# Kernel optimization log

Hardware: AMD Instinct MI355X
Metric: run time of the kernel (lower is better)

## Reference

```python
import jax, jax.numpy as jnp
import numpy as np

EMBED, HEADS, LEVELS, POINTS = 256, 8, 4, 4
HD = EMBED // HEADS
BS, NQ = 2, 16384
SHAPES = [(128, 128), (64, 64), (32, 32), (16, 16)]  # (H, W) per level
NV = sum(h * w for h, w in SHAPES)
EPS = 1e-5


def layernorm(x, g, b):
    mu = jnp.mean(x, -1, keepdims=True)
    var = jnp.mean((x - mu) ** 2, -1, keepdims=True)
    return (x - mu) / jnp.sqrt(var + EPS) * g + b


def bilinear_sample(vl, loc, H, W):
    # vl: (bs, heads, H*W, hd); loc: (bs, nq, heads, P, 2) normalized [0,1]
    # grid_sample semantics: align_corners=False, zero padding
    x = loc[..., 0] * W - 0.5
    y = loc[..., 1] * H - 0.5
    x0 = jnp.floor(x)
    y0 = jnp.floor(y)
    lx, ly = x - x0, y - y0
    x0 = x0.astype(jnp.int32)
    y0 = y0.astype(jnp.int32)
    gather = jax.vmap(jax.vmap(lambda t, i: t[i]))  # over (bs, heads)
    acc = None
    for dx, dy, w in ((0, 0, (1 - lx) * (1 - ly)), (1, 0, lx * (1 - ly)),
                      (0, 1, (1 - lx) * ly), (1, 1, lx * ly)):
        xi, yi = x0 + dx, y0 + dy
        valid = ((xi >= 0) & (xi < W) & (yi >= 0) & (yi < H)).astype(vl.dtype)
        idx = jnp.clip(yi, 0, H - 1) * W + jnp.clip(xi, 0, W - 1)
        idx = idx.transpose(0, 2, 1, 3)           # (bs, heads, nq, P)
        g = gather(vl, idx)                       # (bs, heads, nq, P, hd)
        wv = (w * valid).transpose(0, 2, 1, 3)[..., None]
        acc = g * wv if acc is None else acc + g * wv
    return acc


def forward(lidar_feat, feat_flatten, ref_2d, spatial_shapes, level_start_index,
            q_pose, W_off, b_off, W_attn, b_attn, W_val, b_val, W_out, b_out,
            ln1_g, ln1_b, ffn_w1, ffn_w2, ln2_g, ln2_b):
    identity = lidar_feat                         # (nq, bs, C)
    q = (lidar_feat + q_pose).transpose(1, 0, 2)  # (bs, nq, C)
    bs, nq, C = q.shape
    v = feat_flatten.transpose(1, 0, 2) @ W_val + b_val
    v = v.reshape(bs, -1, HEADS, HD)
    off = (q @ W_off + b_off).reshape(bs, nq, HEADS, LEVELS, POINTS, 2)
    aw = (q @ W_attn + b_attn).reshape(bs, nq, HEADS, LEVELS * POINTS)
    aw = jax.nn.softmax(aw, -1).reshape(bs, nq, HEADS, LEVELS, POINTS)
    ss = np.asarray(spatial_shapes)               # static level shapes
    lsi = np.asarray(level_start_index)
    norm = jnp.asarray(ss[:, ::-1].copy(), q.dtype)  # (L, 2) [W, H]
    loc = ref_2d[:, :, None, :, None, :] + off / norm[None, None, None, :, None, :]
    out = jnp.zeros((bs, nq, HEADS, HD), q.dtype)
    for l in range(LEVELS):
        H, W = int(ss[l, 0]), int(ss[l, 1])
        s = int(lsi[l])
        vl = v[:, s:s + H * W].transpose(0, 2, 1, 3)   # (bs, heads, HW, hd)
        sampled = bilinear_sample(vl, loc[:, :, :, l], H, W)
        out = out + jnp.einsum('bhqpd,bqhp->bqhd', sampled, aw[:, :, :, l, :])
    out = out.reshape(bs, nq, C) @ W_out + b_out
    out = out.transpose(1, 0, 2) + identity       # residual (dropout=eval noop)
    x = layernorm(out, ln1_g, ln1_b)
    x = layernorm(jnp.maximum(x @ ffn_w1, 0.0) @ ffn_w2 + x, ln2_g, ln2_b)
    return x


def setup_inputs():
    key = jax.random.key(0)
    ks = jax.random.split(key, 16)
    starts = np.cumsum([0] + [h * w for h, w in SHAPES])[:-1]
    d = {
        'lidar_feat': jax.random.normal(ks[0], (NQ, BS, EMBED), jnp.float32),
        'feat_flatten': jax.random.normal(ks[1], (NV, BS, EMBED), jnp.float32),
        'ref_2d': jax.random.uniform(ks[2], (BS, NQ, LEVELS, 2), jnp.float32),
        'spatial_shapes': jnp.array(SHAPES, jnp.int32),
        'level_start_index': jnp.array(starts, jnp.int32),
        'q_pose': jax.random.normal(ks[3], (NQ, BS, EMBED), jnp.float32),
        'W_off': 0.02 * jax.random.normal(ks[4], (EMBED, HEADS * LEVELS * POINTS * 2), jnp.float32),
        'b_off': 2.0 * jax.random.normal(ks[5], (HEADS * LEVELS * POINTS * 2,), jnp.float32),
        'W_attn': 0.02 * jax.random.normal(ks[6], (EMBED, HEADS * LEVELS * POINTS), jnp.float32),
        'b_attn': jnp.zeros((HEADS * LEVELS * POINTS,), jnp.float32),
        'W_val': 0.02 * jax.random.normal(ks[7], (EMBED, EMBED), jnp.float32),
        'b_val': jnp.zeros((EMBED,), jnp.float32),
        'W_out': 0.02 * jax.random.normal(ks[8], (EMBED, EMBED), jnp.float32),
        'b_out': jnp.zeros((EMBED,), jnp.float32),
        'ln1_g': jnp.ones((EMBED,), jnp.float32),
        'ln1_b': jnp.zeros((EMBED,), jnp.float32),
        'ffn_w1': 0.02 * jax.random.normal(ks[9], (EMBED, EMBED), jnp.float32),
        'ffn_w2': 0.02 * jax.random.normal(ks[10], (EMBED, EMBED), jnp.float32),
        'ln2_g': jnp.ones((EMBED,), jnp.float32),
        'ln2_b': jnp.zeros((EMBED,), jnp.float32),
    }
    return d


def reference(lidar_feat, feat_flatten, ref_2d, spatial_shapes, level_start_index,
              q_pose, W_off, b_off, W_attn, b_attn, W_val, b_val, W_out, b_out,
              ln1_g, ln1_b, ffn_w1, ffn_w2, ln2_g, ln2_b):
    return forward(lidar_feat, feat_flatten, ref_2d, spatial_shapes,
                   level_start_index, q_pose, W_off, b_off, W_attn, b_attn,
                   W_val, b_val, W_out, b_out, ln1_g, ln1_b, ffn_w1, ffn_w2,
                   ln2_g, ln2_b)
```

## Files before the change

kernel.cpp:

```cpp
#include <hip/hip_runtime.h>
#include <cstdint>

#define EMBED 256
#define HEADS 8
#define LEVELS 4
#define POINTS 4
#define BS 2
#define NQ 16384
#define NV 21760
#define MQ (BS*NQ)
#define MV (BS*NV)
#define VAL_BLK 340
#define OA_BLK  256

typedef __attribute__((ext_vector_type(8))) short short8;
typedef __attribute__((ext_vector_type(4))) float f32x4;
typedef __attribute__((ext_vector_type(2))) float f32x2;

__device__ __forceinline__ unsigned short f2bf(float f) {
    unsigned int u = __float_as_uint(f);
    u = (u + 0x7FFFu + ((u >> 16) & 1u)) >> 16;
    return (unsigned short)u;
}
__device__ __forceinline__ float bf2f(unsigned short h) {
    return __uint_as_float(((unsigned int)h) << 16);
}
__device__ __forceinline__ void glds16(const unsigned short* g, unsigned short* l) {
    __builtin_amdgcn_global_load_lds((const __attribute__((address_space(1))) void*)g,
                                     (__attribute__((address_space(3))) void*)l, 16, 0, 0);
}

struct WtArgs {
    const float* src[6];
    unsigned short* dst[6];
    int n[6];
};
__global__ __launch_bounds__(256) void prep_wt(
    WtArgs a, const float* __restrict__ ref2d, int* __restrict__ bkt)
{
    const int t = threadIdx.x, g = blockIdx.y, bx = blockIdx.x;
    if (g == 6) {
        if (bx < 64) {
#pragma unroll
            for (int i = 0; i < 2; ++i) {
                const int rb = bx * 512 + i * 256 + t;
                const float x = ref2d[(size_t)rb * 8 + 0];
                const float y = ref2d[(size_t)rb * 8 + 1];
                const int qx = min(15, max(0, (int)(x * 16.f)));
                const int qy = min(15, max(0, (int)(y * 16.f)));
                bkt[rb] = (rb >> 14) * 256 + qy * 16 + qx;
            }
        }
        return;
    }
    const int N = a.n[g];
    const int e = bx * 256 + t;
    if (e >= 256 * N) return;
    const int k = e / N, n = e - k * N;
    a.dst[g][(size_t)n * 256 + k] = f2bf(a.src[g][e]);
}

template<int NCOLS>
__device__ __forceinline__ void gemm_core(
    unsigned short* As, unsigned short* Bs, int bx,
    const float* __restrict__ Af, const float* __restrict__ A2f, int inner,
    const unsigned short* __restrict__ Bt,
    const float* __restrict__ bias0, const float* __restrict__ bias1,
    unsigned short* __restrict__ lidarb, unsigned short* __restrict__ outh)
{
    constexpr int FN = NCOLS / 64;
    const int t = threadIdx.x, l = t & 63, w = t >> 6;
    const int wm = w >> 2, wn = w & 3;
    const int frow = l & 15, fgrp = l >> 4;
    const size_t brow = (size_t)bx * 128;

    const int fslot = fgrp ^ ((frow & 3) ^ ((frow >> 2) & 3));
    const int srow = l >> 2;
    const int sswz = (l & 3) ^ ((srow & 3) ^ ((srow >> 2) & 3));
    const unsigned short* gB0 = Bt + ((size_t)(w * 16 + srow)) * 256 + sswz * 8;

    const int arow_s = t >> 2, aslot_s = t & 3;
    const int grow = (int)brow + arow_s;
    const int bidx = grow / inner, nn = grow - bidx * inner;
    const size_t srcrow = (size_t)(nn * BS + bidx) * 256;
    const float* srcA = Af + srcrow;
    const float* srcA2 = A2f ? A2f + srcrow : nullptr;
    const int aswz_s = aslot_s ^ ((arow_s & 3) ^ ((arow_s >> 2) & 3));

    f32x4 acc[4][FN];
#pragma unroll
    for (int i = 0; i < 4; ++i)
#pragma unroll
        for (int j = 0; j < FN; ++j) acc[i][j] = f32x4{0.f, 0.f, 0.f, 0.f};

    float4 pA0 = *(const float4*)(srcA + aslot_s * 8);
    float4 pA1 = *(const float4*)(srcA + aslot_s * 8 + 4);
    float4 pC0, pC1;
    if (srcA2) { pC0 = *(const float4*)(srcA2 + aslot_s * 8);
                 pC1 = *(const float4*)(srcA2 + aslot_s * 8 + 4); }

    for (int k0 = 0; k0 < 256; k0 += 32) {
        glds16(gB0 + k0,         &Bs[w * 512]);
        glds16(gB0 + 32768 + k0, &Bs[(w + 8) * 512]);
        if constexpr (NCOLS == 384)
            glds16(gB0 + 65536 + k0, &Bs[(w + 16) * 512]);

        if (lidarb) {
            short8 lk;
            lk[0] = (short)f2bf(pA0.x); lk[1] = (short)f2bf(pA0.y);
            lk[2] = (short)f2bf(pA0.z); lk[3] = (short)f2bf(pA0.w);
            lk[4] = (short)f2bf(pA1.x); lk[5] = (short)f2bf(pA1.y);
            lk[6] = (short)f2bf(pA1.z); lk[7] = (short)f2bf(pA1.w);
            *reinterpret_cast<short8*>(lidarb + srcrow + k0 + aslot_s * 8) = lk;
        }

        float c[8] = {pA0.x, pA0.y, pA0.z, pA0.w, pA1.x, pA1.y, pA1.z, pA1.w};
        if (srcA2) {
            c[0] += pC0.x; c[1] += pC0.y; c[2] += pC0.z; c[3] += pC0.w;
            c[4] += pC1.x; c[5] += pC1.y; c[6] += pC1.z; c[7] += pC1.w;
        }
        short8 pk;
#pragma unroll
        for (int i = 0; i < 8; ++i) pk[i] = (short)f2bf(c[i]);
        *reinterpret_cast<short8*>(&As[arow_s * 32 + aswz_s * 8]) = pk;
        if (k0 + 32 < 256) {
            pA0 = *(const float4*)(srcA + k0 + 32 + aslot_s * 8);
            pA1 = *(const float4*)(srcA + k0 + 32 + aslot_s * 8 + 4);
            if (srcA2) { pC0 = *(const float4*)(srcA2 + k0 + 32 + aslot_s * 8);
                         pC1 = *(const float4*)(srcA2 + k0 + 32 + aslot_s * 8 + 4); }
        }
        __syncthreads();

        short8 af[4]; short8 bq[FN];
#pragma unroll
        for (int fm = 0; fm < 4; ++fm)
            af[fm] = *reinterpret_cast<const short8*>(&As[(wm * 64 + fm * 16 + frow) * 32 + fslot * 8]);
#pragma unroll
        for (int fn = 0; fn < FN; ++fn)
            bq[fn] = *reinterpret_cast<const short8*>(&Bs[(wn * (NCOLS / 4) + fn * 16 + frow) * 32 + fslot * 8]);
#pragma unroll
        for (int fm = 0; fm < 4; ++fm)
#pragma unroll
            for (int fn = 0; fn < FN; ++fn)
                acc[fm][fn] = __builtin_amdgcn_mfma_f32_16x16x32_bf16(af[fm], bq[fn], acc[fm][fn], 0, 0, 0);
        __syncthreads();
    }

#pragma unroll
    for (int fn = 0; fn < FN; ++fn) {
        const int col = wn * (NCOLS / 4) + fn * 16 + frow;
        float b = 0.f;
        if (NCOLS == 384) b = (col < 256) ? bias0[col] : bias1[col - 256];
        else              b = bias0[col];
#pragma unroll
        for (int fm = 0; fm < 4; ++fm)
#pragma unroll
            for (int j = 0; j < 4; ++j) {
                const size_t row = brow + wm * 64 + fm * 16 + fgrp * 4 + j;
                outh[row * NCOLS + col] = f2bf(acc[fm][fn][j] + b);
            }
    }
}

__global__ __launch_bounds__(512) void valoa_k(
    const float* __restrict__ feat, const float* __restrict__ lidar,
    const float* __restrict__ q_pose,
    const unsigned short* __restrict__ wt_val, const unsigned short* __restrict__ wt_oa,
    const float* __restrict__ b_val, const float* __restrict__ b_off,
    const float* __restrict__ b_attn,
    unsigned short* __restrict__ vb, unsigned short* __restrict__ oa,
    unsigned short* __restrict__ lidarb,
    const int* __restrict__ bkt, int* __restrict__ perm)
{
    __shared__ unsigned short As[128 * 32];
    __shared__ unsigned short Bs[384 * 32];
    const int bx = blockIdx.x;
    if (bx < VAL_BLK) {
        gemm_core<256>(As, Bs, bx, feat, nullptr, NV, wt_val, b_val, nullptr, nullptr, vb);
    } else if (bx < VAL_BLK + OA_BLK) {
        gemm_core<384>(As, Bs, bx - VAL_BLK, lidar, q_pose, NQ, wt_oa, b_off, b_attn, lidarb, oa);
    } else {
        int* hcnt = (int*)As;
        int* cur  = ((int*)As) + 512;
        int* s    = (int*)Bs;
        const int t = threadIdx.x;
        hcnt[t] = 0;
        __syncthreads();
#pragma unroll 4
        for (int i = 0; i < 64; ++i) atomicAdd(&hcnt[bkt[i * 512 + t]], 1);
        __syncthreads();
        const int v = hcnt[t];
        s[t] = v;
        __syncthreads();
        int acc = v;
#pragma unroll
        for (int o = 1; o < 512; o <<= 1) {
            const int add = (t >= o) ? s[t - o] : 0;
            __syncthreads();
            acc += add;
            s[t] = acc;
            __syncthreads();
        }
        cur[t] = acc - v;
        __syncthreads();
#pragma unroll 4
        for (int i = 0; i < 64; ++i) {
            const int rb = i * 512 + t;
            const int pos = atomicAdd(&cur[bkt[rb]], 1);
            perm[pos] = rb;
        }
    }
}

__global__ __launch_bounds__(256) void sampler_k(
    const unsigned short* __restrict__ oa,
    const float* __restrict__ ref2d,
    const unsigned short* __restrict__ v,
    const int* __restrict__ perm,
    unsigned short* __restrict__ outh)
{
    const int bid = blockIdx.x;
    const int sbid = (bid & 7) * (MQ / 4 / 8) + (bid >> 3);
    const int q0 = sbid * 4;
    const int t = threadIdx.x;

    __shared__ __align__(16) uint2 s_d[4][8][74];

#pragma unroll
    for (int it = 0; it < 2; ++it) {
        const int item = t + it * 256;
        const int tq = item >> 7, hlp = item & 127;
        const int h = hlp >> 4, lp = hlp & 15, li = lp >> 2;
        const int rb = perm[q0 + tq];
        const int b = rb >> 14;

        const float2 refv = *(const float2*)(ref2d + (size_t)rb * 8 + li * 2);
        const ushort2 offu = *(const ushort2*)(oa + (size_t)rb * 384 + hlp * 2);
        const float ax = bf2f(oa[(size_t)rb * 384 + 256 + hlp]);

        float m = ax;
#pragma unroll
        for (int o = 1; o < 16; o <<= 1) m = fmaxf(m, __shfl_xor(m, o));
        const float e = __expf(ax - m);
        float sden = e;
#pragma unroll
        for (int o = 1; o < 16; o <<= 1) sden += __shfl_xor(sden, o);
        const float a = e / sden;

        const int Wl[4]  = {128, 64, 32, 16};
        const int S0l[4] = {0, 16384, 20480, 21504};
        const int Wi = Wl[li]; const float Wf = (float)Wi;
        const float x = (refv.x + bf2f(offu.x) / Wf) * Wf - 0.5f;
        const float y = (refv.y + bf2f(offu.y) / Wf) * Wf - 0.5f;
        const float x0f = floorf(x), y0f = floorf(y);
        const float lx = x - x0f, ly = y - y0f;
        const int x0 = (int)x0f, y0 = (int)y0f;
        const float cw[4] = {(1.f - lx) * (1.f - ly) * a, lx * (1.f - ly) * a,
                             (1.f - lx) * ly * a,          lx * ly * a};
        const int base = b * NV + S0l[li];
#pragma unroll
        for (int c = 0; c < 4; ++c) {
            const int xi = x0 + (c & 1), yi = y0 + (c >> 1);
            const bool val = (xi >= 0) & (xi < Wi) & (yi >= 0) & (yi < Wi);
            const int xc = min(max(xi, 0), Wi - 1), yc = min(max(yi, 0), Wi - 1);
            const unsigned int ofs = (unsigned int)(base + yc * Wi + xc) * 256u + h * 32;
            s_d[tq][h][c * 18 + lp] = make_uint2(__float_as_uint(val ? cw[c] : 0.f), ofs);
        }
    }
    __syncthreads();

    const int tq = t >> 6, l = t & 63, h = l >> 3, dq = l & 7;
    const int rb = perm[q0 + tq], b = rb >> 14, qi = rb & (NQ - 1);
    const unsigned short* vd = v + dq * 4;
    const uint2* dp = &s_d[tq][h][0];
    f32x2 acc01 = {0.f, 0.f}, acc23 = {0.f, 0.f};
#pragma unroll
    for (int c = 0; c < 4; ++c) {
#pragma unroll
        for (int i = 0; i < 8; ++i) {
            const uint4 dd = *(const uint4*)(dp + c * 18 + i * 2);
            {
                const uint2 raw = *(const uint2*)(vd + dd.y);
                const float w0 = __uint_as_float(dd.x);
                f32x2 v01; v01.x = __uint_as_float(raw.x << 16);
                           v01.y = __uint_as_float(raw.x & 0xFFFF0000u);
                f32x2 v23; v23.x = __uint_as_float(raw.y << 16);
                           v23.y = __uint_as_float(raw.y & 0xFFFF0000u);
                acc01 += w0 * v01;
                acc23 += w0 * v23;
            }
            {
                const uint2 raw = *(const uint2*)(vd + dd.w);
                const float w1 = __uint_as_float(dd.z);
                f32x2 v01; v01.x = __uint_as_float(raw.x << 16);
                           v01.y = __uint_as_float(raw.x & 0xFFFF0000u);
                f32x2 v23; v23.x = __uint_as_float(raw.y << 16);
                           v23.y = __uint_as_float(raw.y & 0xFFFF0000u);
                acc01 += w1 * v01;
                acc23 += w1 * v23;
            }
        }
    }
    ushort4 o;
    o.x = f2bf(acc01.x); o.y = f2bf(acc01.y);
    o.z = f2bf(acc23.x); o.w = f2bf(acc23.y);
    *(ushort4*)(outh + (size_t)(qi * BS + b) * 256 + h * 32 + dq * 4) = o;
}

__global__ __launch_bounds__(512) void outproj_k(
    const unsigned short* __restrict__ smp, const unsigned short* __restrict__ lidarb,
    const unsigned short* __restrict__ Wo, const float* __restrict__ b_out,
    const float* __restrict__ ln1g, const float* __restrict__ ln1b,
    unsigned short* __restrict__ xln)
{
    __shared__ unsigned short As[128 * 32];
    __shared__ unsigned short Bs[256 * 32];
    __shared__ float2 sdLN[128][4];

    const int t = threadIdx.x, l = t & 63, w = t >> 6;
    const int wm = w >> 2, wn = w & 3;
    const int frow = l & 15, fgrp = l >> 4;
    const size_t brow = (size_t)blockIdx.x * 128;

    const int fslot = fgrp ^ ((frow & 3) ^ ((frow >> 2) & 3));
    const int srow = l >> 2;
    const int sswz = (l & 3) ^ ((srow & 3) ^ ((srow >> 2) & 3));

    const unsigned short* gA = smp + (brow + (size_t)(w * 16 + srow)) * 256 + sswz * 8;
    const unsigned short* gB = Wo + ((size_t)(w * 16 + srow)) * 256 + sswz * 8;

    f32x4 acc[4][4];
#pragma unroll
    for (int i = 0; i < 4; ++i)
#pragma unroll
        for (int j = 0; j < 4; ++j) acc[i][j] = f32x4{0.f, 0.f, 0.f, 0.f};

    for (int k0 = 0; k0 < 256; k0 += 32) {
        glds16(gB + k0,         &Bs[w * 512]);
        glds16(gB + 32768 + k0, &Bs[(w + 8) * 512]);
        glds16(gA + k0, &As[w * 512]);
        __syncthreads();

        short8 af[4], bq[4];
#pragma unroll
        for (int fm = 0; fm < 4; ++fm)
            af[fm] = *reinterpret_cast<const short8*>(&As[(wm * 64 + fm * 16 + frow) * 32 + fslot * 8]);
#pragma unroll
        for (int fn = 0; fn < 4; ++fn)
            bq[fn] = *reinterpret_cast<const short8*>(&Bs[(wn * 64 + fn * 16 + frow) * 32 + fslot * 8]);
#pragma unroll
        for (int fm = 0; fm < 4; ++fm)
#pragma unroll
            for (int fn = 0; fn < 4; ++fn)
                acc[fm][fn] = __builtin_amdgcn_mfma_f32_16x16x32_bf16(af[fm], bq[fn], acc[fm][fn], 0, 0, 0);
        __syncthreads();
    }

    int cols[4];
#pragma unroll
    for (int fn = 0; fn < 4; ++fn) cols[fn] = wn * 64 + fn * 16 + frow;

#pragma unroll
    for (int fm = 0; fm < 4; ++fm)
#pragma unroll
        for (int j = 0; j < 4; ++j) {
            const size_t row = brow + wm * 64 + fm * 16 + fgrp * 4 + j;
#pragma unroll
            for (int fn = 0; fn < 4; ++fn)
                acc[fm][fn][j] += b_out[cols[fn]] + bf2f(lidarb[row * 256 + cols[fn]]);
        }

#pragma unroll
    for (int fm = 0; fm < 4; ++fm)
#pragma unroll
        for (int j = 0; j < 4; ++j) {
            float s1 = 0.f, s2 = 0.f;
#pragma unroll
            for (int fn = 0; fn < 4; ++fn) { const float x = acc[fm][fn][j]; s1 += x; s2 += x * x; }
#pragma unroll
            for (int o = 1; o < 16; o <<= 1) { s1 += __shfl_xor(s1, o); s2 += __shfl_xor(s2, o); }
            if (frow == 0)
                sdLN[wm * 64 + fm * 16 + fgrp * 4 + j][wn] = make_float2(s1, s2);
        }
    __syncthreads();
    float gv[4], bv[4];
#pragma unroll
    for (int fn = 0; fn < 4; ++fn) { gv[fn] = ln1g[cols[fn]]; bv[fn] = ln1b[cols[fn]]; }
#pragma unroll
    for (int fm = 0; fm < 4; ++fm)
#pragma unroll
        for (int j = 0; j < 4; ++j) {
            const int rl = wm * 64 + fm * 16 + fgrp * 4 + j;
            const float2 p0 = sdLN[rl][0], p1 = sdLN[rl][1], p2 = sdLN[rl][2], p3 = sdLN[rl][3];
            const float s1 = p0.x + p1.x + p2.x + p3.x;
            const float s2 = p0.y + p1.y + p2.y + p3.y;
            const float mu = s1 * (1.f / 256.f);
            const float var = s2 * (1.f / 256.f) - mu * mu;
            const float rstd = rsqrtf(var + 1e-5f);
            const size_t row = brow + rl;
#pragma unroll
            for (int fn = 0; fn < 4; ++fn)
                xln[row * 256 + cols[fn]] = f2bf((acc[fm][fn][j] - mu) * rstd * gv[fn] + bv[fn]);
        }
}

__global__ __launch_bounds__(512) void ffn_fused(
    const unsigned short* __restrict__ X,
    const unsigned short* __restrict__ W1t, const unsigned short* __restrict__ W2t,
    const float* __restrict__ lng, const float* __restrict__ lnb,
    float* __restrict__ outf)
{
    __shared__ unsigned short As[64 * 32];
    __shared__ unsigned short Bs[256 * 32];
    __shared__ unsigned short Hs[64 * 256];
    __shared__ float2 sdLN[64][4];

    const int t = threadIdx.x, l = t & 63, w = t >> 6;
    const int wm = w >> 2, wn = w & 3;
    const int frow = l & 15, fgrp = l >> 4;
    const size_t brow = (size_t)blockIdx.x * 64;

    const int fslot = fgrp ^ ((frow & 3) ^ ((frow >> 2) & 3));
    const int srow = l >> 2;
    const int sswz = (l & 3) ^ ((srow & 3) ^ ((srow >> 2) & 3));

    const unsigned short* gX  = X + (brow + (size_t)((w & 3) * 16 + srow)) * 256 + sswz * 8;
    const unsigned short* gW1 = W1t + ((size_t)(w * 16 + srow)) * 256 + sswz * 8;
    const unsigned short* gW2 = W2t + ((size_t)(w * 16 + srow)) * 256 + sswz * 8;

    f32x4 acc[2][4];

#pragma unroll
    for (int i = 0; i < 2; ++i)
#pragma unroll
        for (int j = 0; j < 4; ++j) acc[i][j] = f32x4{0.f, 0.f, 0.f, 0.f};

    for (int k0 = 0; k0 < 256; k0 += 32) {
        glds16(gW1 + k0,         &Bs[w * 512]);
        glds16(gW1 + 32768 + k0, &Bs[(w + 8) * 512]);
        if (w < 4) glds16(gX + k0, &As[w * 512]);
        __syncthreads();

        short8 af[2], bq[4];
#pragma unroll
        for (int fm = 0; fm < 2; ++fm)
            af[fm] = *reinterpret_cast<const short8*>(&As[(wm * 32 + fm * 16 + frow) * 32 + fslot * 8]);
#pragma unroll
        for (int fn = 0; fn < 4; ++fn)
            bq[fn] = *reinterpret_cast<const short8*>(&Bs[(wn * 64 + fn * 16 + frow) * 32 + fslot * 8]);
#pragma unroll
        for (int fm = 0; fm < 2; ++fm)
#pragma unroll
            for (int fn = 0; fn < 4; ++fn)
                acc[fm][fn] = __builtin_amdgcn_mfma_f32_16x16x32_bf16(af[fm], bq[fn], acc[fm][fn], 0, 0, 0);
        __syncthreads();
    }

#pragma unroll
    for (int fm = 0; fm < 2; ++fm)
#pragma unroll
        for (int fn = 0; fn < 4; ++fn) {
            const int col = wn * 64 + fn * 16 + frow;
#pragma unroll
            for (int j = 0; j < 4; ++j) {
                const int row = wm * 32 + fm * 16 + fgrp * 4 + j;
                const int ss = (col >> 3) ^ (row & 7);
                Hs[row * 256 + ss * 8 + (col & 7)] = f2bf(fmaxf(acc[fm][fn][j], 0.f));
            }
        }
    __syncthreads();

#pragma unroll
    for (int i = 0; i < 2; ++i)
#pragma unroll
        for (int j = 0; j < 4; ++j) acc[i][j] = f32x4{0.f, 0.f, 0.f, 0.f};

    for (int k0 = 0; k0 < 256; k0 += 32) {
        glds16(gW2 + k0,         &Bs[w * 512]);
        glds16(gW2 + 32768 + k0, &Bs[(w + 8) * 512]);
        __syncthreads();

        short8 af[2], bq[4];
#pragma unroll
        for (int fm = 0; fm < 2; ++fm) {
            const int row = wm * 32 + fm * 16 + frow;
            const int ksg = (k0 >> 3) + fgrp;
            const int ss = ksg ^ (row & 7);
            af[fm] = *reinterpret_cast<const short8*>(&Hs[row * 256 + ss * 8]);
        }
#pragma unroll
        for (int fn = 0; fn < 4; ++fn)
            bq[fn] = *reinterpret_cast<const short8*>(&Bs[(wn * 64 + fn * 16 + frow) * 32 + fslot * 8]);
#pragma unroll
        for (int fm = 0; fm < 2; ++fm)
#pragma unroll
            for (int fn = 0; fn < 4; ++fn)
                acc[fm][fn] = __builtin_amdgcn_mfma_f32_16x16x32_bf16(af[fm], bq[fn], acc[fm][fn], 0, 0, 0);
        __syncthreads();
    }

#pragma unroll
    for (int fm = 0; fm < 2; ++fm)
#pragma unroll
        for (int fn = 0; fn < 4; ++fn) {
            const int col = wn * 64 + fn * 16 + frow;
#pragma unroll
            for (int j = 0; j < 4; ++j) {
                const size_t row = brow + wm * 32 + fm * 16 + fgrp * 4 + j;
                acc[fm][fn][j] += bf2f(X[row * 256 + col]);
            }
        }
#pragma unroll
    for (int fm = 0; fm < 2; ++fm)
#pragma unroll
        for (int j = 0; j < 4; ++j) {
            float s1 = 0.f, s2 = 0.f;
#pragma unroll
            for (int fn = 0; fn < 4; ++fn) { const float x = acc[fm][fn][j]; s1 += x; s2 += x * x; }
#pragma unroll
            for (int o = 1; o < 16; o <<= 1) { s1 += __shfl_xor(s1, o); s2 += __shfl_xor(s2, o); }
            if (frow == 0)
                sdLN[wm * 32 + fm * 16 + fgrp * 4 + j][wn] = make_float2(s1, s2);
        }
    __syncthreads();
#pragma unroll
    for (int fm = 0; fm < 2; ++fm)
#pragma unroll
        for (int j = 0; j < 4; ++j) {
            const int rl = wm * 32 + fm * 16 + fgrp * 4 + j;
            const float2 p0 = sdLN[rl][0], p1 = sdLN[rl][1], p2 = sdLN[rl][2], p3 = sdLN[rl][3];
            const float s1 = p0.x + p1.x + p2.x + p3.x;
            const float s2 = p0.y + p1.y + p2.y + p3.y;
            const float mu = s1 * (1.f / 256.f);
            const float var = s2 * (1.f / 256.f) - mu * mu;
            const float rstd = rsqrtf(var + 1e-5f);
            const size_t row = brow + rl;
#pragma unroll
            for (int fn = 0; fn < 4; ++fn) {
                const int col = wn * 64 + fn * 16 + frow;
                outf[row * 256 + col] = (acc[fm][fn][j] - mu) * rstd * lng[col] + lnb[col];
            }
        }
}

extern "C" void kernel_launch(void* const* d_in, const int* in_sizes, int n_in,
                              void* d_out, int out_size, void* d_ws, size_t ws_size,
                              hipStream_t stream)
{
    const float* lidar  = (const float*)d_in[0];
    const float* feat   = (const float*)d_in[1];
    const float* ref2d  = (const float*)d_in[2];
    const float* q_pose = (const float*)d_in[5];
    const float* W_off  = (const float*)d_in[6];
    const float* b_off  = (const float*)d_in[7];
    const float* W_attn = (const float*)d_in[8];
    const float* b_attn = (const float*)d_in[9];
    const float* W_val  = (const float*)d_in[10];
    const float* b_val  = (const float*)d_in[11];
    const float* W_out  = (const float*)d_in[12];
    const float* b_out  = (const float*)d_in[13];
    const float* ln1_g  = (const float*)d_in[14];
    const float* ln1_b  = (const float*)d_in[15];
    const float* ffn_w1 = (const float*)d_in[16];
    const float* ffn_w2 = (const float*)d_in[17];
    const float* ln2_g  = (const float*)d_in[18];
    const float* ln2_b  = (const float*)d_in[19];

    float* out = (float*)d_out;
    char*  ws  = (char*)d_ws;

    unsigned short* vb     = (unsigned short*)(ws + 0);
    unsigned short* oa     = (unsigned short*)(ws + 22282240);
    unsigned short* smp    = (unsigned short*)(ws + 47448064);
    unsigned short* xln    = (unsigned short*)(ws + 64225280);
    unsigned short* lidarb = (unsigned short*)(ws + 81002496);
    unsigned short* wt     = (unsigned short*)(ws + 97779712);
    int* perm = (int*)(ws + 98500608);
    int* bkt  = (int*)(ws + 98631680);
    unsigned short* wt_val = wt;
    unsigned short* wt_oa  = wt + 65536;
    unsigned short* wt_out = wt + 163840;
    unsigned short* wt_f1  = wt + 229376;
    unsigned short* wt_f2  = wt + 294912;

    WtArgs wa;
    wa.src[0] = W_val;  wa.dst[0] = wt_val;          wa.n[0] = 256;
    wa.src[1] = W_off;  wa.dst[1] = wt_oa;           wa.n[1] = 256;
    wa.src[2] = W_attn; wa.dst[2] = wt_oa + 65536;   wa.n[2] = 128;
    wa.src[3] = W_out;  wa.dst[3] = wt_out;          wa.n[3] = 256;
    wa.src[4] = ffn_w1; wa.dst[4] = wt_f1;           wa.n[4] = 256;
    wa.src[5] = ffn_w2; wa.dst[5] = wt_f2;           wa.n[5] = 256;

    prep_wt<<<dim3(384, 7), dim3(256), 0, stream>>>(wa, ref2d, bkt);

    valoa_k<<<dim3(VAL_BLK + OA_BLK + 1), dim3(512), 0, stream>>>(
        feat, lidar, q_pose, wt_val, wt_oa, b_val, b_off, b_attn,
        vb, oa, lidarb, bkt, perm);

    sampler_k<<<dim3(MQ / 4), dim3(256), 0, stream>>>(oa, ref2d, vb, perm, smp);

    outproj_k<<<dim3(MQ / 128), dim3(512), 0, stream>>>(
        smp, lidarb, wt_out, b_out, ln1_g, ln1_b, xln);

    ffn_fused<<<dim3(MQ / 64), dim3(512), 0, stream>>>(
        xln, wt_f1, wt_f2, ln2_g, ln2_b, out);
}
```

Before: 195.2 us.

## Pre-convert GEMM inputs to bf16 in prep kernel and load A via LDS DMA

Adds a separate pass in the prep kernel that converts feat, lidar and lidar+q_pose to bf16 row-major buffers. This lets the value and offset/attention GEMMs stream A tiles with global_load_lds instead of loading fp32, converting in registers and storing to LDS. The bucket histogram now builds with global atomics during prep, so the single sort block only does the scan and scatter. The cost is an extra full read and write of the inputs in bf16 plus a memset, traded for a simpler, more latency-tolerant GEMM main loop.

```diff
diff --git a/kernel.cpp b/kernel.cpp
--- a/kernel.cpp
+++ b/kernel.cpp
@@ -13,6 +13,11 @@
 #define VAL_BLK 340
 #define OA_BLK  256
 
+#define WT_B  2304
+#define BKT_B 2368
+#define FB_B  13248
+#define QB_B  21440
+
 typedef __attribute__((ext_vector_type(8))) short short8;
 typedef __attribute__((ext_vector_type(4))) float f32x4;
 typedef __attribute__((ext_vector_type(2))) float f32x2;
@@ -35,38 +40,65 @@
     unsigned short* dst[6];
     int n[6];
 };
-__global__ __launch_bounds__(256) void prep_wt(
-    WtArgs a, const float* __restrict__ ref2d, int* __restrict__ bkt)
+__global__ __launch_bounds__(256) void prep_k(
+    WtArgs a, const float* __restrict__ ref2d,
+    const float* __restrict__ feat, const float* __restrict__ lidar,
+    const float* __restrict__ q_pose,
+    unsigned short* __restrict__ featb, unsigned short* __restrict__ qb,
+    unsigned short* __restrict__ lidarb,
+    int* __restrict__ bkt, int* __restrict__ hist)
 {
-    const int t = threadIdx.x, g = blockIdx.y, bx = blockIdx.x;
-    if (g == 6) {
-        if (bx < 64) {
-#pragma unroll
-            for (int i = 0; i < 2; ++i) {
-                const int rb = bx * 512 + i * 256 + t;
-                const float x = ref2d[(size_t)rb * 8 + 0];
-                const float y = ref2d[(size_t)rb * 8 + 1];
-                const int qx = min(15, max(0, (int)(x * 16.f)));
-                const int qy = min(15, max(0, (int)(y * 16.f)));
-                bkt[rb] = (rb >> 14) * 256 + qy * 16 + qx;
-            }
-        }
-        return;
-    }
-    const int N = a.n[g];
-    const int e = bx * 256 + t;
-    if (e >= 256 * N) return;
-    const int k = e / N, n = e - k * N;
-    a.dst[g][(size_t)n * 256 + k] = f2bf(a.src[g][e]);
+    const int bx = blockIdx.x, t = threadIdx.x;
+    if (bx < WT_B) {
+        const int g = bx / 384;
+        const int e = (bx - g * 384) * 256 + t;
+        const int N = a.n[g];
+        if (e < 256 * N) {
+            const int k = e / N, n = e - k * N;
+            a.dst[g][(size_t)n * 256 + k] = f2bf(a.src[g][e]);
+        }
+    } else if (bx < BKT_B) {
+        const int base = (bx - WT_B) * 512;
+#pragma unroll
+        for (int i = 0; i < 2; ++i) {
+            const int rb = base + i * 256 + t;
+            const float x = ref2d[(size_t)rb * 8 + 0];
+            const float y = ref2d[(size_t)rb * 8 + 1];
+            const int qx = min(15, max(0, (int)(x * 16.f)));
+            const int qy = min(15, max(0, (int)(y * 16.f)));
+            const int bv = (rb >> 14) * 256 + qy * 16 + qx;
+            bkt[rb] = bv;
+            atomicAdd(&hist[bv], 1);
+        }
+    } else if (bx < FB_B) {
+        const int r = (bx - BKT_B) * 4 + (t >> 6);
+        const int c = (t & 63) * 4;
+        const int b = r / NV, n = r - b * NV;
+        const float4 v4 = *(const float4*)(feat + (size_t)(n * BS + b) * 256 + c);
+        ushort4 o; o.x = f2bf(v4.x); o.y = f2bf(v4.y); o.z = f2bf(v4.z); o.w = f2bf(v4.w);
+        *(ushort4*)(featb + (size_t)r * 256 + c) = o;
+    } else {
+        const int r = (bx - FB_B) * 4 + (t >> 6);
+        const int c = (t & 63) * 4;
+        const int b = r >> 14, n = r & (NQ - 1);
+        const size_t src = (size_t)(n * BS + b) * 256 + c;
+        const float4 lv = *(const float4*)(lidar + src);
+        const float4 qv = *(const float4*)(q_pose + src);
+        ushort4 lo; lo.x = f2bf(lv.x); lo.y = f2bf(lv.y); lo.z = f2bf(lv.z); lo.w = f2bf(lv.w);
+        *(ushort4*)(lidarb + src) = lo;
+        ushort4 qo;
+        qo.x = f2bf(lv.x + qv.x); qo.y = f2bf(lv.y + qv.y);
+        qo.z = f2bf(lv.z + qv.z); qo.w = f2bf(lv.w + qv.w);
+        *(ushort4*)(qb + (size_t)r * 256 + c) = qo;
+    }
 }
 
 template<int NCOLS>
-__device__ __forceinline__ void gemm_core(
+__device__ __forceinline__ void gemm_bf(
     unsigned short* As, unsigned short* Bs, int bx,
-    const float* __restrict__ Af, const float* __restrict__ A2f, int inner,
-    const unsigned short* __restrict__ Bt,
+    const unsigned short* __restrict__ A, const unsigned short* __restrict__ Bt,
     const float* __restrict__ bias0, const float* __restrict__ bias1,
-    unsigned short* __restrict__ lidarb, unsigned short* __restrict__ outh)
+    unsigned short* __restrict__ outh)
 {
     constexpr int FN = NCOLS / 64;
     const int t = threadIdx.x, l = t & 63, w = t >> 6;
@@ -77,15 +109,9 @@
     const int fslot = fgrp ^ ((frow & 3) ^ ((frow >> 2) & 3));
     const int srow = l >> 2;
     const int sswz = (l & 3) ^ ((srow & 3) ^ ((srow >> 2) & 3));
-    const unsigned short* gB0 = Bt + ((size_t)(w * 16 + srow)) * 256 + sswz * 8;
-
-    const int arow_s = t >> 2, aslot_s = t & 3;
-    const int grow = (int)brow + arow_s;
-    const int bidx = grow / inner, nn = grow - bidx * inner;
-    const size_t srcrow = (size_t)(nn * BS + bidx) * 256;
-    const float* srcA = Af + srcrow;
-    const float* srcA2 = A2f ? A2f + srcrow : nullptr;
-    const int aswz_s = aslot_s ^ ((arow_s & 3) ^ ((arow_s >> 2) & 3));
+
+    const unsigned short* gA = A + (brow + (size_t)(w * 16 + srow)) * 256 + sswz * 8;
+    const unsigned short* gB = Bt + ((size_t)(w * 16 + srow)) * 256 + sswz * 8;
 
     f32x4 acc[4][FN];
 #pragma unroll
@@ -93,42 +119,12 @@
 #pragma unroll
         for (int j = 0; j < FN; ++j) acc[i][j] = f32x4{0.f, 0.f, 0.f, 0.f};
 
-    float4 pA0 = *(const float4*)(srcA + aslot_s * 8);
-    float4 pA1 = *(const float4*)(srcA + aslot_s * 8 + 4);
-    float4 pC0, pC1;
-    if (srcA2) { pC0 = *(const float4*)(srcA2 + aslot_s * 8);
-                 pC1 = *(const float4*)(srcA2 + aslot_s * 8 + 4); }
-
     for (int k0 = 0; k0 < 256; k0 += 32) {
-        glds16(gB0 + k0,         &Bs[w * 512]);
-        glds16(gB0 + 32768 + k0, &Bs[(w + 8) * 512]);
+        glds16(gB + k0,         &Bs[w * 512]);
+        glds16(gB + 32768 + k0, &Bs[(w + 8) * 512]);
         if constexpr (NCOLS == 384)
-            glds16(gB0 + 65536 + k0, &Bs[(w + 16) * 512]);
-
-        if (lidarb) {
-            short8 lk;
-            lk[0] = (short)f2bf(pA0.x); lk[1] = (short)f2bf(pA0.y);
-            lk[2] = (short)f2bf(pA0.z); lk[3] = (short)f2bf(pA0.w);
-            lk[4] = (short)f2bf(pA1.x); lk[5] = (short)f2bf(pA1.y);
-            lk[6] = (short)f2bf(pA1.z); lk[7] = (short)f2bf(pA1.w);
-            *reinterpret_cast<short8*>(lidarb + srcrow + k0 + aslot_s * 8) = lk;
-        }
-
-        float c[8] = {pA0.x, pA0.y, pA0.z, pA0.w, pA1.x, pA1.y, pA1.z, pA1.w};
-        if (srcA2) {
-            c[0] += pC0.x; c[1] += pC0.y; c[2] += pC0.z; c[3] += pC0.w;
-            c[4] += pC1.x; c[5] += pC1.y; c[6] += pC1.z; c[7] += pC1.w;
-        }
-        short8 pk;
-#pragma unroll
-        for (int i = 0; i < 8; ++i) pk[i] = (short)f2bf(c[i]);
-        *reinterpret_cast<short8*>(&As[arow_s * 32 + aswz_s * 8]) = pk;
-        if (k0 + 32 < 256) {
-            pA0 = *(const float4*)(srcA + k0 + 32 + aslot_s * 8);
-            pA1 = *(const float4*)(srcA + k0 + 32 + aslot_s * 8 + 4);
-            if (srcA2) { pC0 = *(const float4*)(srcA2 + k0 + 32 + aslot_s * 8);
-                         pC1 = *(const float4*)(srcA2 + k0 + 32 + aslot_s * 8 + 4); }
-        }
+            glds16(gB + 65536 + k0, &Bs[(w + 16) * 512]);
+        glds16(gA + k0, &As[w * 512]);
         __syncthreads();
 
         short8 af[4]; short8 bq[FN];
@@ -149,7 +145,7 @@
 #pragma unroll
     for (int fn = 0; fn < FN; ++fn) {
         const int col = wn * (NCOLS / 4) + fn * 16 + frow;
-        float b = 0.f;
+        float b;
         if (NCOLS == 384) b = (col < 256) ? bias0[col] : bias1[col - 256];
         else              b = bias0[col];
 #pragma unroll
@@ -163,33 +159,26 @@
 }
 
 __global__ __launch_bounds__(512) void valoa_k(
-    const float* __restrict__ feat, const float* __restrict__ lidar,
-    const float* __restrict__ q_pose,
+    const unsigned short* __restrict__ featb, const unsigned short* __restrict__ qb,
     const unsigned short* __restrict__ wt_val, const unsigned short* __restrict__ wt_oa,
     const float* __restrict__ b_val, const float* __restrict__ b_off,
     const float* __restrict__ b_attn,
     unsigned short* __restrict__ vb, unsigned short* __restrict__ oa,
-    unsigned short* __restrict__ lidarb,
-    const int* __restrict__ bkt, int* __restrict__ perm)
+    const int* __restrict__ hist, const int* __restrict__ bkt,
+    int* __restrict__ perm)
 {
     __shared__ unsigned short As[128 * 32];
     __shared__ unsigned short Bs[384 * 32];
     const int bx = blockIdx.x;
     if (bx < VAL_BLK) {
-        gemm_core<256>(As, Bs, bx, feat, nullptr, NV, wt_val, b_val, nullptr, nullptr, vb);
+        gemm_bf<256>(As, Bs, bx, featb, wt_val, b_val, nullptr, vb);
     } else if (bx < VAL_BLK + OA_BLK) {
-        gemm_core<384>(As, Bs, bx - VAL_BLK, lidar, q_pose, NQ, wt_oa, b_off, b_attn, lidarb, oa);
+        gemm_bf<384>(As, Bs, bx - VAL_BLK, qb, wt_oa, b_off, b_attn, oa);
     } else {
-        int* hcnt = (int*)As;
-        int* cur  = ((int*)As) + 512;
-        int* s    = (int*)Bs;
+        int* s   = (int*)As;
+        int* cur = ((int*)As) + 512;
         const int t = threadIdx.x;
-        hcnt[t] = 0;
-        __syncthreads();
-#pragma unroll 4
-        for (int i = 0; i < 64; ++i) atomicAdd(&hcnt[bkt[i * 512 + t]], 1);
-        __syncthreads();
-        const int v = hcnt[t];
+        const int v = hist[t];
         s[t] = v;
         __syncthreads();
         int acc = v;
@@ -572,11 +561,14 @@
     unsigned short* vb     = (unsigned short*)(ws + 0);
     unsigned short* oa     = (unsigned short*)(ws + 22282240);
     unsigned short* smp    = (unsigned short*)(ws + 47448064);
+    unsigned short* qb     = smp;
     unsigned short* xln    = (unsigned short*)(ws + 64225280);
-    unsigned short* lidarb = (unsigned short*)(ws + 81002496);
-    unsigned short* wt     = (unsigned short*)(ws + 97779712);
-    int* perm = (int*)(ws + 98500608);
-    int* bkt  = (int*)(ws + 98631680);
+    unsigned short* featb  = xln;
+    unsigned short* lidarb = (unsigned short*)(ws + 86507520);
+    unsigned short* wt     = (unsigned short*)(ws + 103284736);
+    int* perm = (int*)(ws + 104005632);
+    int* bkt  = (int*)(ws + 104136704);
+    int* hist = (int*)(ws + 104267776);
     unsigned short* wt_val = wt;
     unsigned short* wt_oa  = wt + 65536;
     unsigned short* wt_out = wt + 163840;
@@ -591,11 +583,14 @@
     wa.src[4] = ffn_w1; wa.dst[4] = wt_f1;           wa.n[4] = 256;
     wa.src[5] = ffn_w2; wa.dst[5] = wt_f2;           wa.n[5] = 256;
 
-    prep_wt<<<dim3(384, 7), dim3(256), 0, stream>>>(wa, ref2d, bkt);
+    hipMemsetAsync(hist, 0, 2048, stream);
+
+    prep_k<<<dim3(QB_B), dim3(256), 0, stream>>>(
+        wa, ref2d, feat, lidar, q_pose, featb, qb, lidarb, bkt, hist);
 
     valoa_k<<<dim3(VAL_BLK + OA_BLK + 1), dim3(512), 0, stream>>>(
-        feat, lidar, q_pose, wt_val, wt_oa, b_val, b_off, b_attn,
-        vb, oa, lidarb, bkt, perm);
+        featb, qb, wt_val, wt_oa, b_val, b_off, b_attn,
+        vb, oa, hist, bkt, perm);
 
     sampler_k<<<dim3(MQ / 4), dim3(256), 0, stream>>>(oa, ref2d, vb, perm, smp);
 
```

New measurement: 211.9 us. +8.6%, slower.

## Shrink value/offset GEMM tiles to 32 rows and precompute bucket histogram

Applied to the files above, without the earlier changes.

The fused value/offset-attention projection GEMM now uses 32-row tiles with 256-thread blocks instead of 128-row tiles with 512 threads. This gives about four times as many blocks for better CU occupancy and load balance. The query bucket histogram moves into the prep kernel via global atomics, so the sort block in valoa_k only runs a prefix scan and scatter. The trade-offs are that B tiles are reloaded by more blocks, the new histogram buffer needs an extra memset, and there is global atomic contention.

```diff
diff --git a/kernel.cpp b/kernel.cpp
--- a/kernel.cpp
+++ b/kernel.cpp
@@ -10,8 +10,8 @@
 #define NV 21760
 #define MQ (BS*NQ)
 #define MV (BS*NV)
-#define VAL_BLK 340
-#define OA_BLK  256
+#define VAL32 1360
+#define OA32  1024
 
 typedef __attribute__((ext_vector_type(8))) short short8;
 typedef __attribute__((ext_vector_type(4))) float f32x4;
@@ -36,7 +36,8 @@
     int n[6];
 };
 __global__ __launch_bounds__(256) void prep_wt(
-    WtArgs a, const float* __restrict__ ref2d, int* __restrict__ bkt)
+    WtArgs a, const float* __restrict__ ref2d,
+    int* __restrict__ bkt, int* __restrict__ hist)
 {
     const int t = threadIdx.x, g = blockIdx.y, bx = blockIdx.x;
     if (g == 6) {
@@ -48,7 +49,9 @@
                 const float y = ref2d[(size_t)rb * 8 + 1];
                 const int qx = min(15, max(0, (int)(x * 16.f)));
                 const int qy = min(15, max(0, (int)(y * 16.f)));
-                bkt[rb] = (rb >> 14) * 256 + qy * 16 + qx;
+                const int bv = (rb >> 14) * 256 + qy * 16 + qx;
+                bkt[rb] = bv;
+                atomicAdd(&hist[bv], 1);
             }
         }
         return;
@@ -61,7 +64,7 @@
 }
 
 template<int NCOLS>
-__device__ __forceinline__ void gemm_core(
+__device__ __forceinline__ void gemm32(
     unsigned short* As, unsigned short* Bs, int bx,
     const float* __restrict__ Af, const float* __restrict__ A2f, int inner,
     const unsigned short* __restrict__ Bt,
@@ -70,76 +73,65 @@
 {
     constexpr int FN = NCOLS / 64;
     const int t = threadIdx.x, l = t & 63, w = t >> 6;
-    const int wm = w >> 2, wn = w & 3;
     const int frow = l & 15, fgrp = l >> 4;
-    const size_t brow = (size_t)bx * 128;
+    const size_t brow = (size_t)bx * 32;
 
     const int fslot = fgrp ^ ((frow & 3) ^ ((frow >> 2) & 3));
     const int srow = l >> 2;
     const int sswz = (l & 3) ^ ((srow & 3) ^ ((srow >> 2) & 3));
     const unsigned short* gB0 = Bt + ((size_t)(w * 16 + srow)) * 256 + sswz * 8;
 
-    const int arow_s = t >> 2, aslot_s = t & 3;
-    const int grow = (int)brow + arow_s;
+    const int arow = t >> 3;
+    const int acol = (t & 7) * 4;
+    const int grow = (int)brow + arow;
     const int bidx = grow / inner, nn = grow - bidx * inner;
     const size_t srcrow = (size_t)(nn * BS + bidx) * 256;
     const float* srcA = Af + srcrow;
     const float* srcA2 = A2f ? A2f + srcrow : nullptr;
-    const int aswz_s = aslot_s ^ ((arow_s & 3) ^ ((arow_s >> 2) & 3));
-
-    f32x4 acc[4][FN];
-#pragma unroll
-    for (int i = 0; i < 4; ++i)
+    const int aslot = (t & 7) >> 1, ahalf = t & 1;
+    const int aswz = aslot ^ ((arow & 3) ^ ((arow >> 2) & 3));
+    const int aoff = arow * 32 + aswz * 8 + ahalf * 4;
+
+    f32x4 acc[2][FN];
+#pragma unroll
+    for (int i = 0; i < 2; ++i)
 #pragma unroll
         for (int j = 0; j < FN; ++j) acc[i][j] = f32x4{0.f, 0.f, 0.f, 0.f};
 
-    float4 pA0 = *(const float4*)(srcA + aslot_s * 8);
-    float4 pA1 = *(const float4*)(srcA + aslot_s * 8 + 4);
-    float4 pC0, pC1;
-    if (srcA2) { pC0 = *(const float4*)(srcA2 + aslot_s * 8);
-                 pC1 = *(const float4*)(srcA2 + aslot_s * 8 + 4); }
+    float4 pA = *(const float4*)(srcA + acol);
+    float4 pC;
+    if (srcA2) pC = *(const float4*)(srcA2 + acol);
 
     for (int k0 = 0; k0 < 256; k0 += 32) {
-        glds16(gB0 + k0,         &Bs[w * 512]);
-        glds16(gB0 + 32768 + k0, &Bs[(w + 8) * 512]);
-        if constexpr (NCOLS == 384)
-            glds16(gB0 + 65536 + k0, &Bs[(w + 16) * 512]);
+#pragma unroll
+        for (int c = 0; c < FN; ++c)
+            glds16(gB0 + c * 16384 + k0, &Bs[(c * 4 + w) * 512]);
 
         if (lidarb) {
-            short8 lk;
-            lk[0] = (short)f2bf(pA0.x); lk[1] = (short)f2bf(pA0.y);
-            lk[2] = (short)f2bf(pA0.z); lk[3] = (short)f2bf(pA0.w);
-            lk[4] = (short)f2bf(pA1.x); lk[5] = (short)f2bf(pA1.y);
-            lk[6] = (short)f2bf(pA1.z); lk[7] = (short)f2bf(pA1.w);
-            *reinterpret_cast<short8*>(lidarb + srcrow + k0 + aslot_s * 8) = lk;
-        }
-
-        float c[8] = {pA0.x, pA0.y, pA0.z, pA0.w, pA1.x, pA1.y, pA1.z, pA1.w};
-        if (srcA2) {
-            c[0] += pC0.x; c[1] += pC0.y; c[2] += pC0.z; c[3] += pC0.w;
-            c[4] += pC1.x; c[5] += pC1.y; c[6] += pC1.z; c[7] += pC1.w;
-        }
-        short8 pk;
-#pragma unroll
-        for (int i = 0; i < 8; ++i) pk[i] = (short)f2bf(c[i]);
-        *reinterpret_cast<short8*>(&As[arow_s * 32 + aswz_s * 8]) = pk;
+            ushort4 lk;
+            lk.x = f2bf(pA.x); lk.y = f2bf(pA.y); lk.z = f2bf(pA.z); lk.w = f2bf(pA.w);
+            *(ushort4*)(lidarb + srcrow + k0 + acol) = lk;
+        }
+        float c0 = pA.x, c1 = pA.y, c2 = pA.z, c3 = pA.w;
+        if (srcA2) { c0 += pC.x; c1 += pC.y; c2 += pC.z; c3 += pC.w; }
+        ushort4 pk; pk.x = f2bf(c0); pk.y = f2bf(c1); pk.z = f2bf(c2); pk.w = f2bf(c3);
+        *(ushort4*)(&As[aoff]) = pk;
+
         if (k0 + 32 < 256) {
-            pA0 = *(const float4*)(srcA + k0 + 32 + aslot_s * 8);
-            pA1 = *(const float4*)(srcA + k0 + 32 + aslot_s * 8 + 4);
-            if (srcA2) { pC0 = *(const float4*)(srcA2 + k0 + 32 + aslot_s * 8);
-                         pC1 = *(const float4*)(srcA2 + k0 + 32 + aslot_s * 8 + 4); }
-        }
-        __syncthreads();
-
-        short8 af[4]; short8 bq[FN];
-#pragma unroll
-        for (int fm = 0; fm < 4; ++fm)
-            af[fm] = *reinterpret_cast<const short8*>(&As[(wm * 64 + fm * 16 + frow) * 32 + fslot * 8]);
+            pA = *(const float4*)(srcA + k0 + 32 + acol);
+            if (srcA2) pC = *(const float4*)(srcA2 + k0 + 32 + acol);
+        }
+        __syncthreads();
+
+        short8 af[2]; short8 bq[FN];
+#pragma unroll
+        for (int fm = 0; fm < 2; ++fm)
+            af[fm] = *reinterpret_cast<const short8*>(&As[(fm * 16 + frow) * 32 + fslot * 8]);
 #pragma unroll
         for (int fn = 0; fn < FN; ++fn)
-            bq[fn] = *reinterpret_cast<const short8*>(&Bs[(wn * (NCOLS / 4) + fn * 16 + frow) * 32 + fslot * 8]);
-#pragma unroll
-        for (int fm = 0; fm < 4; ++fm)
+            bq[fn] = *reinterpret_cast<const short8*>(&Bs[(w * (NCOLS / 4) + fn * 16 + frow) * 32 + fslot * 8]);
+#pragma unroll
+        for (int fm = 0; fm < 2; ++fm)
 #pragma unroll
             for (int fn = 0; fn < FN; ++fn)
                 acc[fm][fn] = __builtin_amdgcn_mfma_f32_16x16x32_bf16(af[fm], bq[fn], acc[fm][fn], 0, 0, 0);
@@ -148,21 +140,21 @@
 
 #pragma unroll
     for (int fn = 0; fn < FN; ++fn) {
-        const int col = wn * (NCOLS / 4) + fn * 16 + frow;
-        float b = 0.f;
+        const int col = w * (NCOLS / 4) + fn * 16 + frow;
+        float b;
         if (NCOLS == 384) b = (col < 256) ? bias0[col] : bias1[col - 256];
         else              b = bias0[col];
 #pragma unroll
-        for (int fm = 0; fm < 4; ++fm)
+        for (int fm = 0; fm < 2; ++fm)
 #pragma unroll
             for (int j = 0; j < 4; ++j) {
-                const size_t row = brow + wm * 64 + fm * 16 + fgrp * 4 + j;
+                const size_t row = brow + fm * 16 + fgrp * 4 + j;
                 outh[row * NCOLS + col] = f2bf(acc[fm][fn][j] + b);
             }
     }
 }
 
-__global__ __launch_bounds__(512) void valoa_k(
+__global__ __launch_bounds__(256) void valoa_k(
     const float* __restrict__ feat, const float* __restrict__ lidar,
     const float* __restrict__ q_pose,
     const unsigned short* __restrict__ wt_val, const unsigned short* __restrict__ wt_oa,
@@ -170,42 +162,40 @@
     const float* __restrict__ b_attn,
     unsigned short* __restrict__ vb, unsigned short* __restrict__ oa,
     unsigned short* __restrict__ lidarb,
-    const int* __restrict__ bkt, int* __restrict__ perm)
+    const int* __restrict__ hist, const int* __restrict__ bkt,
+    int* __restrict__ perm)
 {
-    __shared__ unsigned short As[128 * 32];
+    __shared__ unsigned short As[32 * 32];
     __shared__ unsigned short Bs[384 * 32];
     const int bx = blockIdx.x;
-    if (bx < VAL_BLK) {
-        gemm_core<256>(As, Bs, bx, feat, nullptr, NV, wt_val, b_val, nullptr, nullptr, vb);
-    } else if (bx < VAL_BLK + OA_BLK) {
-        gemm_core<384>(As, Bs, bx - VAL_BLK, lidar, q_pose, NQ, wt_oa, b_off, b_attn, lidarb, oa);
+    if (bx < VAL32) {
+        gemm32<256>(As, Bs, bx, feat, nullptr, NV, wt_val, b_val, nullptr, nullptr, vb);
+    } else if (bx < VAL32 + OA32) {
+        gemm32<384>(As, Bs, bx - VAL32, lidar, q_pose, NQ, wt_oa, b_off, b_attn, lidarb, oa);
     } else {
-        int* hcnt = (int*)As;
-        int* cur  = ((int*)As) + 512;
-        int* s    = (int*)Bs;
+        int* ps  = (int*)As;
+        int* cur = (int*)Bs;
         const int t = threadIdx.x;
-        hcnt[t] = 0;
-        __syncthreads();
-#pragma unroll 4
-        for (int i = 0; i < 64; ++i) atomicAdd(&hcnt[bkt[i * 512 + t]], 1);
-        __syncthreads();
-        const int v = hcnt[t];
-        s[t] = v;
-        __syncthreads();
-        int acc = v;
-#pragma unroll
-        for (int o = 1; o < 512; o <<= 1) {
-            const int add = (t >= o) ? s[t - o] : 0;
+        const int2 hv = ((const int2*)hist)[t];
+        const int pair = hv.x + hv.y;
+        ps[t] = pair;
+        __syncthreads();
+        int acc = pair;
+#pragma unroll
+        for (int o = 1; o < 256; o <<= 1) {
+            const int add = (t >= o) ? ps[t - o] : 0;
             __syncthreads();
             acc += add;
-            s[t] = acc;
+            ps[t] = acc;
             __syncthreads();
         }
-        cur[t] = acc - v;
+        const int excl = acc - pair;
+        cur[2 * t]     = excl;
+        cur[2 * t + 1] = excl + hv.x;
         __syncthreads();
 #pragma unroll 4
-        for (int i = 0; i < 64; ++i) {
-            const int rb = i * 512 + t;
+        for (int i = 0; i < 128; ++i) {
+            const int rb = i * 256 + t;
             const int pos = atomicAdd(&cur[bkt[rb]], 1);
             perm[pos] = rb;
         }
@@ -577,6 +567,7 @@
     unsigned short* wt     = (unsigned short*)(ws + 97779712);
     int* perm = (int*)(ws + 98500608);
     int* bkt  = (int*)(ws + 98631680);
+    int* hist = (int*)(ws + 98762752);
     unsigned short* wt_val = wt;
     unsigned short* wt_oa  = wt + 65536;
     unsigned short* wt_out = wt + 163840;
@@ -591,11 +582,13 @@
     wa.src[4] = ffn_w1; wa.dst[4] = wt_f1;           wa.n[4] = 256;
     wa.src[5] = ffn_w2; wa.dst[5] = wt_f2;           wa.n[5] = 256;
 
-    prep_wt<<<dim3(384, 7), dim3(256), 0, stream>>>(wa, ref2d, bkt);
-
-    valoa_k<<<dim3(VAL_BLK + OA_BLK + 1), dim3(512), 0, stream>>>(
+    hipMemsetAsync(hist, 0, 2048, stream);
+
+    prep_wt<<<dim3(384, 7), dim3(256), 0, stream>>>(wa, ref2d, bkt, hist);
+
+    valoa_k<<<dim3(VAL32 + OA32 + 1), dim3(256), 0, stream>>>(
         feat, lidar, q_pose, wt_val, wt_oa, b_val, b_off, b_attn,
-        vb, oa, lidarb, bkt, perm);
+        vb, oa, lidarb, hist, bkt, perm);
 
     sampler_k<<<dim3(MQ / 4), dim3(256), 0, stream>>>(oa, ref2d, vb, perm, smp);
 
```

Result: slower. 207.8 us (+6.5%).
